# Kernel optimization log

Measured on AMD Instinct MI355X. Metric: run time of the kernel, lower is better.

Reference implementation:

```python
import jax, jax.numpy as jnp
import numpy as np

N_NODES = 100000
N_EDGES = 1600000
F_IN, F_HID, F_OUT = 64, 64, 32


def setup_inputs() -> dict:
    key = jax.random.key(0)
    k1, k2, k3, k4 = jax.random.split(key, 4)
    x = jax.random.normal(k1, (N_NODES, F_IN), dtype=jnp.float32)
    edge_idx = jax.random.randint(k2, (2, N_EDGES), 0, N_NODES, dtype=jnp.int64)
    W1 = jax.random.normal(k3, (F_IN, F_HID), dtype=jnp.float32) * (1.0 / np.sqrt(F_IN))
    b1 = jnp.zeros((F_HID,), dtype=jnp.float32)
    W2 = jax.random.normal(k4, (F_HID, F_OUT), dtype=jnp.float32) * (1.0 / np.sqrt(F_HID))
    b2 = jnp.zeros((F_OUT,), dtype=jnp.float32)
    return {"x": x, "edge_idx": edge_idx, "W1": W1, "b1": b1, "W2": W2, "b2": b2}


def _gcn_conv(h, src, dst, norm, W, b, n):
    # PyG GCNConv: transform first, then normalized sum aggregation, then bias.
    h = h @ W                                   # [N, F_out]
    msg = h[src] * norm[:, None]                # [E+N, F_out] gather + scale
    agg = jax.ops.segment_sum(msg, dst, num_segments=n)  # scatter-add
    return agg + b


def reference(x, edge_idx, W1, b1, W2, b2):
    n = x.shape[0]
    loop = jnp.arange(n, dtype=edge_idx.dtype)
    src = jnp.concatenate([edge_idx[0], loop])  # add self-loops
    dst = jnp.concatenate([edge_idx[1], loop])
    # symmetric normalization D^-1/2 (A+I) D^-1/2
    deg = jax.ops.segment_sum(jnp.ones_like(dst, dtype=x.dtype), dst, num_segments=n)
    dinv = jnp.where(deg > 0, jax.lax.rsqrt(deg), 0.0)
    norm = dinv[src] * dinv[dst]                # [E+N]

    h = _gcn_conv(x, src, dst, norm, W1, b1, n)
    h = jax.nn.relu(h)
    # dropout(p=0.5) is identity in eval mode (deterministic reference)
    out = _gcn_conv(h, src, dst, norm, W2, b2, n)
    return out
```

## Files before the change

kernel.cpp:

```cpp
#include <hip/hip_runtime.h>
#include <hip/hip_bf16.h>
#include <hip/hip_fp16.h>


#define N_FEAT_IN 64
#define B2SHIFT 9
#define CHUNK 4096

struct alignas(8) half4 { __half2 lo, hi; };

__global__ __launch_bounds__(1024) void passA_hist(const int* __restrict__ dst,
                                                   int* __restrict__ H, int E) {
    __shared__ int h[256];
    int t = threadIdx.x;
    if (t < 256) h[t] = 0;
    __syncthreads();
    int base = blockIdx.x * CHUNK;
    int end = min(base + CHUNK, E);
    for (int i = base + t; i < end; i += 1024)
        atomicAdd(&h[dst[i] >> B2SHIFT], 1);
    __syncthreads();
    if (t < 256) H[blockIdx.x * 256 + t] = h[t];
}

__global__ __launch_bounds__(512) void col_scan_a(int* __restrict__ H,
                                                  int* __restrict__ ctot, int NR) {
    __shared__ int s[512];
    int b = blockIdx.x;
    int t = threadIdx.x;
    int v = (t < NR) ? H[t * 256 + b] : 0;
    s[t] = v;
    __syncthreads();
    for (int off = 1; off < 512; off <<= 1) {
        int a = (t >= off) ? s[t - off] : 0;
        __syncthreads();
        s[t] += a;
        __syncthreads();
    }
    if (t < NR) H[t * 256 + b] = s[t] - v;
    if (t == 511) ctot[b] = s[511];
}

__global__ __launch_bounds__(256) void col_scan_b(const int* __restrict__ ctot,
                                                  int* __restrict__ cbase,
                                                  int* __restrict__ bbase,
                                                  int* __restrict__ row_ptr,
                                                  int NB, int n, int E) {
    __shared__ int s[256];
    int t = threadIdx.x;
    int v = ctot[t];
    s[t] = v;
    __syncthreads();
    for (int off = 1; off < 256; off <<= 1) {
        int a = (t >= off) ? s[t - off] : 0;
        __syncthreads();
        s[t] += a;
        __syncthreads();
    }
    int e = s[t] - v;
    cbase[t] = e;
    if (t < NB) bbase[t] = e;
    if (t == 0) { bbase[NB] = E; row_ptr[n] = E; }
}

__global__ __launch_bounds__(1024) void passB_place(const int* __restrict__ src,
                                                    const int* __restrict__ dst,
                                                    const int* __restrict__ H,
                                                    const int* __restrict__ cbase,
                                                    unsigned* __restrict__ bedges, int E) {
    __shared__ int cur[256];
    int t = threadIdx.x;
    if (t < 256) cur[t] = H[blockIdx.x * 256 + t] + cbase[t];
    __syncthreads();
    int base = blockIdx.x * CHUNK;
    int end = min(base + CHUNK, E);
    for (int i = base + t; i < end; i += 1024) {
        int d = dst[i];
        int p = atomicAdd(&cur[d >> B2SHIFT], 1);
        bedges[p] = ((unsigned)src[i] << B2SHIFT) | (unsigned)(d & 511);
    }
}

__global__ __launch_bounds__(1024) void bucket_csr(const int* __restrict__ bbase,
                                                   const unsigned* __restrict__ bedges,
                                                   int* __restrict__ row_ptr,
                                                   float* __restrict__ dinv,
                                                   int* __restrict__ csr_src, int n) {
    __shared__ int lh[512];
    __shared__ int cur[512];
    int t = threadIdx.x;
    if (t < 512) lh[t] = 0;
    __syncthreads();
    int b = blockIdx.x;
    int beg = bbase[b], end = bbase[b + 1];
    for (int i = beg + t; i < end; i += 1024)
        atomicAdd(&lh[bedges[i] & 511], 1);
    __syncthreads();
    int c = (t < 512) ? lh[t] : 0;
    for (int off = 1; off < 512; off <<= 1) {
        int a = (t < 512 && t >= off) ? lh[t - off] : 0;
        __syncthreads();
        if (t < 512) lh[t] += a;
        __syncthreads();
    }
    if (t < 512) {
        int d = (b << B2SHIFT) + t;
        int excl = beg + lh[t] - c;
        cur[t] = excl;
        if (d < n) {
            row_ptr[d] = excl;
            dinv[d] = rsqrtf((float)c + 1.0f);
        }
    }
    __syncthreads();
    for (int i = beg + t; i < end; i += 1024) {
        unsigned v = bedges[i];
        int p = atomicAdd(&cur[v & 511], 1);
        csr_src[p] = (int)(v >> B2SHIFT);
    }
}

__global__ __launch_bounds__(256) void gemm64(const float* __restrict__ A,
                                              const float* __restrict__ W,
                                              const float* __restrict__ dinv,
                                              __half* __restrict__ outh, int n) {
    constexpr int K = 64, FO = 64, CPT = 16;
    __shared__ float As[64][K + 4];
    __shared__ float Ws[K][FO];

    const int t = threadIdx.x;
    const int r0 = blockIdx.x * 64;

    if (blockIdx.x == 0 && t < FO)
        outh[(size_t)n * FO + t] = __float2half(0.f);

    for (int i = t; i < K * FO / 4; i += 256) {
        int k = i / (FO / 4);
        int c4 = (i % (FO / 4)) * 4;
        *(float4*)&Ws[k][c4] = *(const float4*)&W[k * FO + c4];
    }
    for (int i = t; i < 1024; i += 256) {
        int row = i / 16;
        int c4 = (i % 16) * 4;
        int g = r0 + row;
        float4 v = make_float4(0.f, 0.f, 0.f, 0.f);
        if (g < n) v = *(const float4*)&A[(size_t)g * K + c4];
        *(float4*)&As[row][c4] = v;
    }
    __syncthreads();

    const int row = t >> 2;
    const int c0 = (t & 3) * CPT;
    float acc[CPT];
#pragma unroll
    for (int j = 0; j < CPT; ++j) acc[j] = 0.f;
#pragma unroll
    for (int k = 0; k < K; ++k) {
        float xv = As[row][k];
#pragma unroll
        for (int j = 0; j < CPT; ++j) acc[j] = fmaf(xv, Ws[k][c0 + j], acc[j]);
    }

    int g = r0 + row;
    if (g < n) {
        float sc = dinv[g];
#pragma unroll
        for (int j4 = 0; j4 < CPT; j4 += 4) {
            half4 h;
            h.lo = __floats2half2_rn(acc[j4] * sc, acc[j4 + 1] * sc);
            h.hi = __floats2half2_rn(acc[j4 + 2] * sc, acc[j4 + 3] * sc);
            *(half4*)&outh[(size_t)g * FO + c0 + j4] = h;
        }
    }
}

__global__ __launch_bounds__(256) void agg64_fused(const int* __restrict__ row_ptr,
                                                   const int* __restrict__ csr_src,
                                                   const float* __restrict__ dinv,
                                                   const __half* __restrict__ xs1,
                                                   const float* __restrict__ b1,
                                                   const float* __restrict__ W2,
                                                   __half* __restrict__ xs2, int n) {
    __shared__ float Wsh[64][33];
    __shared__ float b1s[64];
    __shared__ float trow[4][64];
    int t = threadIdx.x;
    for (int i = t; i < 64 * 32; i += 256) Wsh[i >> 5][i & 31] = W2[i];
    if (t < 64) b1s[t] = b1[t];
    __syncthreads();

    if (blockIdx.x == 0 && t < 32) xs2[(size_t)n * 32 + t] = __float2half(0.f);

    int d = __builtin_amdgcn_readfirstlane(blockIdx.x * 4 + (t >> 6));
    if (d >= n) return;
    int lane = t & 63;

    int beg = row_ptr[d];
    int end = row_ptr[d + 1];
    float acc = __half2float(xs1[(size_t)d * 64 + lane]);

    for (int jb = beg; jb < end; jb += 8) {
        int idx[8];
#pragma unroll
        for (int k = 0; k < 8; ++k) {
            int j = jb + k;
            int s = csr_src[min(j, end - 1)];
            idx[k] = __builtin_amdgcn_readfirstlane((j < end) ? s : n);
        }
        float v[8];
#pragma unroll
        for (int k = 0; k < 8; ++k)
            v[k] = __half2float(xs1[(size_t)idx[k] * 64 + lane]);
        acc += ((v[0] + v[1]) + (v[2] + v[3])) + ((v[4] + v[5]) + (v[6] + v[7]));
    }

    float di = dinv[d];
    float tv = fmaxf(fmaf(di, acc, b1s[lane]), 0.f);

    int w = t >> 6;
    trow[w][lane] = tv;

    float s = 0.f;
    int c = lane & 31;
    int k0 = (lane >> 5) * 32;
#pragma unroll
    for (int k = 0; k < 32; ++k)
        s = fmaf(trow[w][k0 + k], Wsh[k0 + k][c], s);
    s += __shfl_xor(s, 32);

    if (lane < 32)
        xs2[(size_t)d * 32 + c] = __float2half(di * s);
}

__global__ __launch_bounds__(256) void agg32(const int* __restrict__ row_ptr,
                                             const int* __restrict__ csr_src,
                                             const float* __restrict__ dinv,
                                             const __half* __restrict__ xs2,
                                             const float* __restrict__ bias,
                                             float* __restrict__ out, int n) {
    int d = blockIdx.x * 8 + (threadIdx.x >> 5);
    int f = threadIdx.x & 31;
    if (d >= n) return;

    int beg = row_ptr[d];
    int end = row_ptr[d + 1];
    float acc = __half2float(xs2[(size_t)d * 32 + f]);

    for (int jb = beg; jb < end; jb += 8) {
        int idx[8];
#pragma unroll
        for (int k = 0; k < 8; ++k) {
            int j = jb + k;
            int s = csr_src[min(j, end - 1)];
            idx[k] = (j < end) ? s : n;
        }
        float v[8];
#pragma unroll
        for (int k = 0; k < 8; ++k)
            v[k] = __half2float(xs2[(size_t)idx[k] * 32 + f]);
        acc += ((v[0] + v[1]) + (v[2] + v[3])) + ((v[4] + v[5]) + (v[6] + v[7]));
    }

    out[(size_t)d * 32 + f] = dinv[d] * acc + bias[f];
}

extern "C" void kernel_launch(void* const* d_in, const int* in_sizes, int n_in,
                              void* d_out, int out_size, void* d_ws, size_t ws_size,
                              hipStream_t stream) {
    const float* x  = (const float*)d_in[0];
    const int*   ei = (const int*)d_in[1];
    const float* W1 = (const float*)d_in[2];
    const float* b1 = (const float*)d_in[3];
    const float* W2 = (const float*)d_in[4];
    const float* b2 = (const float*)d_in[5];
    float* out = (float*)d_out;

    const int n = in_sizes[0] / N_FEAT_IN;
    const int E = in_sizes[1] / 2;
    const int* srcI = ei;
    const int* dstI = ei + E;

    const int NB = (n + 511) >> B2SHIFT;
    const int NR = (E + CHUNK - 1) / CHUNK;

    char* ws = (char*)d_ws;
    size_t off = 0;
    auto alloc = [&](size_t bytes) {
        void* p = ws + off;
        off += (bytes + 255) & ~(size_t)255;
        return p;
    };
    float*    dinv    = (float*)alloc((size_t)n * 4);
    int*      row_ptr = (int*)alloc((size_t)(n + 1) * 4);
    int*      bbase   = (int*)alloc((size_t)(NB + 1) * 4);
    int*      ctot    = (int*)alloc((size_t)256 * 4);
    int*      cbase   = (int*)alloc((size_t)256 * 4);
    int*      H       = (int*)alloc((size_t)NR * 256 * 4);
    unsigned* bedges  = (unsigned*)alloc((size_t)E * 4);
    int*      csr_src = (int*)alloc((size_t)E * 4);
    __half*   xs1     = (__half*)alloc((size_t)(n + 1) * 64 * 2);
    __half*   xs2     = (__half*)alloc((size_t)(n + 1) * 32 * 2);

    passA_hist<<<NR, 1024, 0, stream>>>(dstI, H, E);
    col_scan_a<<<256, 512, 0, stream>>>(H, ctot, NR);
    col_scan_b<<<1, 256, 0, stream>>>(ctot, cbase, bbase, row_ptr, NB, n, E);
    passB_place<<<NR, 1024, 0, stream>>>(srcI, dstI, H, cbase, bedges, E);

    bucket_csr<<<NB, 1024, 0, stream>>>(bbase, bedges, row_ptr, dinv, csr_src, n);

    gemm64<<<(n + 63) / 64, 256, 0, stream>>>(x, W1, dinv, xs1, n);

    agg64_fused<<<(n + 3) / 4, 256, 0, stream>>>(row_ptr, csr_src, dinv, xs1,
                                                 b1, W2, xs2, n);

    agg32<<<(n + 7) / 8, 256, 0, stream>>>(row_ptr, csr_src, dinv, xs2, b2, out, n);
}
```

Baseline: 234.3 us.

## Unfuse layer-2 GEMM from aggregation and vectorize gathers with half4 per thread

Splits the fused aggregate+GEMM kernel into a standalone 64-wide aggregation that writes a relu'd fp16 hidden buffer and a separate tiled GEMM kernel for W2. Both aggregation kernels now process several destination rows per wavefront, with each thread gathering 4 halves (8 bytes) per neighbor instead of one half per lane. The aim is fewer, wider gather loads and freedom from the per-block W2 shared-memory setup and LDS matvec. In exchange it adds an extra kernel launch and a round trip of the hidden activations through global memory.

```diff
diff --git a/kernel.cpp b/kernel.cpp
--- a/kernel.cpp
+++ b/kernel.cpp
@@ -174,30 +174,22 @@
     }
 }
 
-__global__ __launch_bounds__(256) void agg64_fused(const int* __restrict__ row_ptr,
-                                                   const int* __restrict__ csr_src,
-                                                   const float* __restrict__ dinv,
-                                                   const __half* __restrict__ xs1,
-                                                   const float* __restrict__ b1,
-                                                   const float* __restrict__ W2,
-                                                   __half* __restrict__ xs2, int n) {
-    __shared__ float Wsh[64][33];
-    __shared__ float b1s[64];
-    __shared__ float trow[4][64];
-    int t = threadIdx.x;
-    for (int i = t; i < 64 * 32; i += 256) Wsh[i >> 5][i & 31] = W2[i];
-    if (t < 64) b1s[t] = b1[t];
-    __syncthreads();
-
-    if (blockIdx.x == 0 && t < 32) xs2[(size_t)n * 32 + t] = __float2half(0.f);
-
-    int d = __builtin_amdgcn_readfirstlane(blockIdx.x * 4 + (t >> 6));
+__global__ __launch_bounds__(256) void agg64(const int* __restrict__ row_ptr,
+                                             const int* __restrict__ csr_src,
+                                             const float* __restrict__ dinv,
+                                             const __half* __restrict__ xs1,
+                                             const float* __restrict__ b1,
+                                             __half* __restrict__ th, int n) {
+    int d = blockIdx.x * 16 + (threadIdx.x >> 4);
     if (d >= n) return;
-    int lane = t & 63;
+    int c = threadIdx.x & 15;
 
     int beg = row_ptr[d];
     int end = row_ptr[d + 1];
-    float acc = __half2float(xs1[(size_t)d * 64 + lane]);
+
+    half4 sv = *(const half4*)&xs1[(size_t)d * 64 + 4 * c];
+    float2 slo = __half22float2(sv.lo), shi = __half22float2(sv.hi);
+    float a0 = slo.x, a1 = slo.y, a2 = shi.x, a3 = shi.y;
 
     for (int jb = beg; jb < end; jb += 8) {
         int idx[8];
@@ -205,46 +197,105 @@
         for (int k = 0; k < 8; ++k) {
             int j = jb + k;
             int s = csr_src[min(j, end - 1)];
-            idx[k] = __builtin_amdgcn_readfirstlane((j < end) ? s : n);
-        }
-        float v[8];
+            idx[k] = (j < end) ? s : n;
+        }
+        half4 v[8];
 #pragma unroll
         for (int k = 0; k < 8; ++k)
-            v[k] = __half2float(xs1[(size_t)idx[k] * 64 + lane]);
-        acc += ((v[0] + v[1]) + (v[2] + v[3])) + ((v[4] + v[5]) + (v[6] + v[7]));
+            v[k] = *(const half4*)&xs1[(size_t)idx[k] * 64 + 4 * c];
+#pragma unroll
+        for (int k = 0; k < 8; ++k) {
+            float2 lo = __half22float2(v[k].lo), hi = __half22float2(v[k].hi);
+            a0 += lo.x; a1 += lo.y; a2 += hi.x; a3 += hi.y;
+        }
     }
 
     float di = dinv[d];
-    float tv = fmaxf(fmaf(di, acc, b1s[lane]), 0.f);
-
-    int w = t >> 6;
-    trow[w][lane] = tv;
-
-    float s = 0.f;
-    int c = lane & 31;
-    int k0 = (lane >> 5) * 32;
-#pragma unroll
-    for (int k = 0; k < 32; ++k)
-        s = fmaf(trow[w][k0 + k], Wsh[k0 + k][c], s);
-    s += __shfl_xor(s, 32);
-
-    if (lane < 32)
-        xs2[(size_t)d * 32 + c] = __float2half(di * s);
+    float4 bv = *(const float4*)&b1[4 * c];
+    float t0 = fmaxf(fmaf(di, a0, bv.x), 0.f);
+    float t1 = fmaxf(fmaf(di, a1, bv.y), 0.f);
+    float t2 = fmaxf(fmaf(di, a2, bv.z), 0.f);
+    float t3 = fmaxf(fmaf(di, a3, bv.w), 0.f);
+    half4 h;
+    h.lo = __floats2half2_rn(t0, t1);
+    h.hi = __floats2half2_rn(t2, t3);
+    *(half4*)&th[(size_t)d * 64 + 4 * c] = h;
+}
+
+__global__ __launch_bounds__(256) void gemm32h(const __half* __restrict__ Ah,
+                                               const float* __restrict__ W,
+                                               const float* __restrict__ dinv,
+                                               __half* __restrict__ outh, int n) {
+    constexpr int K = 64, FO = 32, CPT = 8;
+    __shared__ float As[64][K + 4];
+    __shared__ float Ws[K][FO];
+
+    const int t = threadIdx.x;
+    const int r0 = blockIdx.x * 64;
+
+    if (blockIdx.x == 0 && t < FO)
+        outh[(size_t)n * FO + t] = __float2half(0.f);
+
+    for (int i = t; i < K * FO / 4; i += 256) {
+        int k = i / (FO / 4);
+        int c4 = (i % (FO / 4)) * 4;
+        *(float4*)&Ws[k][c4] = *(const float4*)&W[k * FO + c4];
+    }
+    for (int i = t; i < 1024; i += 256) {
+        int row = i / 16;
+        int c4 = (i % 16) * 4;
+        int g = r0 + row;
+        float4 v = make_float4(0.f, 0.f, 0.f, 0.f);
+        if (g < n) {
+            half4 hv = *(const half4*)&Ah[(size_t)g * K + c4];
+            float2 lo = __half22float2(hv.lo), hi = __half22float2(hv.hi);
+            v = make_float4(lo.x, lo.y, hi.x, hi.y);
+        }
+        *(float4*)&As[row][c4] = v;
+    }
+    __syncthreads();
+
+    const int row = t >> 2;
+    const int c0 = (t & 3) * CPT;
+    float acc[CPT];
+#pragma unroll
+    for (int j = 0; j < CPT; ++j) acc[j] = 0.f;
+#pragma unroll
+    for (int k = 0; k < K; ++k) {
+        float xv = As[row][k];
+#pragma unroll
+        for (int j = 0; j < CPT; ++j) acc[j] = fmaf(xv, Ws[k][c0 + j], acc[j]);
+    }
+
+    int g = r0 + row;
+    if (g < n) {
+        float sc = dinv[g];
+#pragma unroll
+        for (int j4 = 0; j4 < CPT; j4 += 4) {
+            half4 h;
+            h.lo = __floats2half2_rn(acc[j4] * sc, acc[j4 + 1] * sc);
+            h.hi = __floats2half2_rn(acc[j4 + 2] * sc, acc[j4 + 3] * sc);
+            *(half4*)&outh[(size_t)g * FO + c0 + j4] = h;
+        }
+    }
 }
 
 __global__ __launch_bounds__(256) void agg32(const int* __restrict__ row_ptr,
                                              const int* __restrict__ csr_src,
                                              const float* __restrict__ dinv,
                                              const __half* __restrict__ xs2,
-                                             const float* __restrict__ bias,
+                                             const float* __restrict__ b2,
                                              float* __restrict__ out, int n) {
-    int d = blockIdx.x * 8 + (threadIdx.x >> 5);
-    int f = threadIdx.x & 31;
+    int d = blockIdx.x * 32 + (threadIdx.x >> 3);
     if (d >= n) return;
+    int c = threadIdx.x & 7;
 
     int beg = row_ptr[d];
     int end = row_ptr[d + 1];
-    float acc = __half2float(xs2[(size_t)d * 32 + f]);
+
+    half4 sv = *(const half4*)&xs2[(size_t)d * 32 + 4 * c];
+    float2 slo = __half22float2(sv.lo), shi = __half22float2(sv.hi);
+    float a0 = slo.x, a1 = slo.y, a2 = shi.x, a3 = shi.y;
 
     for (int jb = beg; jb < end; jb += 8) {
         int idx[8];
@@ -254,14 +305,25 @@
             int s = csr_src[min(j, end - 1)];
             idx[k] = (j < end) ? s : n;
         }
-        float v[8];
+        half4 v[8];
 #pragma unroll
         for (int k = 0; k < 8; ++k)
-            v[k] = __half2float(xs2[(size_t)idx[k] * 32 + f]);
-        acc += ((v[0] + v[1]) + (v[2] + v[3])) + ((v[4] + v[5]) + (v[6] + v[7]));
-    }
-
-    out[(size_t)d * 32 + f] = dinv[d] * acc + bias[f];
+            v[k] = *(const half4*)&xs2[(size_t)idx[k] * 32 + 4 * c];
+#pragma unroll
+        for (int k = 0; k < 8; ++k) {
+            float2 lo = __half22float2(v[k].lo), hi = __half22float2(v[k].hi);
+            a0 += lo.x; a1 += lo.y; a2 += hi.x; a3 += hi.y;
+        }
+    }
+
+    float di = dinv[d];
+    float4 bv = *(const float4*)&b2[4 * c];
+    float4 r;
+    r.x = fmaf(di, a0, bv.x);
+    r.y = fmaf(di, a1, bv.y);
+    r.z = fmaf(di, a2, bv.z);
+    r.w = fmaf(di, a3, bv.w);
+    *(float4*)&out[(size_t)d * 32 + 4 * c] = r;
 }
 
 extern "C" void kernel_launch(void* const* d_in, const int* in_sizes, int n_in,
@@ -299,6 +361,7 @@
     unsigned* bedges  = (unsigned*)alloc((size_t)E * 4);
     int*      csr_src = (int*)alloc((size_t)E * 4);
     __half*   xs1     = (__half*)alloc((size_t)(n + 1) * 64 * 2);
+    __half*   th      = (__half*)alloc((size_t)n * 64 * 2);
     __half*   xs2     = (__half*)alloc((size_t)(n + 1) * 32 * 2);
 
     passA_hist<<<NR, 1024, 0, stream>>>(dstI, H, E);
@@ -310,8 +373,9 @@
 
     gemm64<<<(n + 63) / 64, 256, 0, stream>>>(x, W1, dinv, xs1, n);
 
-    agg64_fused<<<(n + 3) / 4, 256, 0, stream>>>(row_ptr, csr_src, dinv, xs1,
-                                                 b1, W2, xs2, n);
-
-    agg32<<<(n + 7) / 8, 256, 0, stream>>>(row_ptr, csr_src, dinv, xs2, b2, out, n);
-}
+    agg64<<<(n + 15) / 16, 256, 0, stream>>>(row_ptr, csr_src, dinv, xs1, b1, th, n);
+
+    gemm32h<<<(n + 63) / 64, 256, 0, stream>>>(th, W2, dinv, xs2, n);
+
+    agg32<<<(n + 31) / 32, 256, 0, stream>>>(row_ptr, csr_src, dinv, xs2, b2, out, n);
+}
```

Result: faster. 202.7 us (-13.5%).
